# Performance work log

Measured on AMD Instinct MI355X. Metric: run time of the kernel, lower is better.

## Reference

```python
import jax, jax.numpy as jnp
import numpy as np

D_MODEL = 1024
N_HEADS = 16
D_K = D_MODEL // N_HEADS
SEQ = 2048
BATCH = 2
THETA = 10000.0


def apply_rope(x, positions, theta):
    # x: [..., h, s, d_k], positions: [s]
    d_k = x.shape[-1]
    inv_freq = 1.0 / (theta ** (jnp.arange(0, d_k, 2, dtype=jnp.float32) / d_k))  # [d_k/2]
    ang = positions.astype(jnp.float32)[:, None] * inv_freq[None, :]  # [s, d_k/2]
    cos, sin = jnp.cos(ang), jnp.sin(ang)
    xe, xo = x[..., 0::2], x[..., 1::2]
    re = xe * cos - xo * sin
    ro = xe * sin + xo * cos
    return jnp.stack([re, ro], axis=-1).reshape(x.shape)


def setup_inputs() -> dict:
    key = jax.random.key(0)
    ks = jax.random.split(key, 7)
    f = lambda k, s: jax.random.normal(k, s, dtype=jnp.float32)
    return {
        "Q": f(ks[0], (BATCH, SEQ, D_MODEL)),
        "K": f(ks[1], (BATCH, SEQ, D_MODEL)),
        "V": f(ks[2], (BATCH, SEQ, D_MODEL)),
        "w_q": f(ks[3], (D_MODEL, D_MODEL)) * 0.02,
        "w_k": f(ks[4], (D_MODEL, D_MODEL)) * 0.02,
        "w_v": f(ks[5], (D_MODEL, D_MODEL)) * 0.02,
        "w_o": f(ks[6], (D_MODEL, D_MODEL)) * 0.02,
        "mask": jnp.tril(jnp.ones((SEQ, SEQ), dtype=bool)),
        "token_positions": jnp.arange(SEQ, dtype=jnp.int32),
    }


def reference(Q, K, V, w_q, w_k, w_v, w_o, mask, token_positions):
    h, d_k = N_HEADS, D_K
    # projections: weight is [h*d_k, d_model], applied as x @ W^T
    def proj(x, w):
        y = jnp.einsum('bsd,ed->bse', x, w)
        b, s, _ = y.shape
        return y.reshape(b, s, h, d_k).transpose(0, 2, 1, 3)  # [b,h,s,d_k]
    q = proj(Q, w_q)
    k = proj(K, w_k)
    v = proj(V, w_v)
    q = apply_rope(q, token_positions, THETA)
    k = apply_rope(k, token_positions, THETA)
    scores = jnp.einsum('bhqd,bhkd->bhqk', q, k) / jnp.sqrt(jnp.float32(d_k))
    scores = jnp.where(mask, scores, -jnp.inf)
    attn = jax.nn.softmax(scores, axis=-1)
    out = jnp.einsum('bhqk,bhkd->bhqd', attn, v)
    b, _, s, _ = out.shape
    out = out.transpose(0, 2, 1, 3).reshape(b, s, h * d_k)
    return jnp.einsum('bse,de->bsd', out, w_o)
```

## Files before the change

### kernel.cpp

```cpp
#include <hip/hip_runtime.h>

#define SEQ 2048
#define BATCH 2
#define DM 1024
#define NH 16
#define DK 64
#define BH (BATCH*NH)

typedef __attribute__((ext_vector_type(8))) short bf16x8;
typedef __attribute__((ext_vector_type(4))) float f32x4;

__device__ __forceinline__ ushort f2bf(float f) {
  union { float f; unsigned u; } v; v.f = f;
  unsigned r = (v.u + 0x7fffu + ((v.u >> 16) & 1u)) >> 16;
  return (ushort)r;
}
__device__ __forceinline__ float bf2f(ushort h) {
  union { unsigned u; float f; } v; v.u = ((unsigned)h) << 16;
  return v.f;
}
__device__ __forceinline__ unsigned cvtpk(float lo, float hi) {
  unsigned r;
  asm("v_cvt_pk_bf16_f32 %0, %1, %2" : "=v"(r) : "v"(lo), "v"(hi));
  return r;
}

#define WAITV6 asm volatile("s_waitcnt vmcnt(6)" ::: "memory")
#define WAITV3 asm volatile("s_waitcnt vmcnt(3)" ::: "memory")
#define WAITV0 asm volatile("s_waitcnt vmcnt(0)" ::: "memory")
#define WAITL0 asm volatile("s_waitcnt lgkmcnt(0)" ::: "memory")
#define BARR() __builtin_amdgcn_s_barrier()

struct P4 { const float* p0; const float* p1; const float* p2; const float* p3; };
__global__ void k_castN(P4 in, ushort* __restrict__ out, int n4) {
  const float* src = (blockIdx.z == 0) ? in.p0 : (blockIdx.z == 1) ? in.p1
                    : (blockIdx.z == 2) ? in.p2 : in.p3;
  ushort* dst = out + (size_t)blockIdx.z * (size_t)n4 * 4;
  int i = blockIdx.x * blockDim.x + threadIdx.x;
  int st = gridDim.x * blockDim.x;
  for (; i < n4; i += st) {
    float4 v = reinterpret_cast<const float4*>(src)[i];
    ushort4 o;
    o.x = f2bf(v.x); o.y = f2bf(v.y); o.z = f2bf(v.z); o.w = f2bf(v.w);
    reinterpret_cast<ushort4*>(dst)[i] = o;
  }
}

__global__ void k_rope_tab(float* __restrict__ tab) {
  int id = blockIdx.x * blockDim.x + threadIdx.x;
  if (id >= SEQ * 32) return;
  int s = id >> 5, i = id & 31;
  float inv = powf(10000.f, -(float)i / 32.f);
  float ang = (float)s * inv;
  float sn, cs;
  sincosf(ang, &sn, &cs);
  tab[id * 2] = cs;
  tab[id * 2 + 1] = sn;
}

__device__ __forceinline__ void gll16(const void* g, void* l) {
  __builtin_amdgcn_global_load_lds((const __attribute__((address_space(1))) void*)g,
                                   (__attribute__((address_space(3))) void*)l, 16, 0, 0);
}

#define GSTAGE(AD, BD, kk_) do {                                               \
    _Pragma("unroll")                                                          \
    for (int i_ = 0; i_ < 4; ++i_) {                                           \
      int tt_ = i_ * 256 + tid;                                                \
      int row_ = tt_ >> 3, c_ = (tt_ & 7) ^ (row_ & 7);                        \
      gll16(Afp + (size_t)(m0 + row_) * K + (kk_) + c_ * 4,                    \
            (void*)((char*)(AD) + (i_ * 256 + w * 64) * 16));                  \
    }                                                                          \
    gll16(Bw + (size_t)(n0 + w * 16 + lrow) * K + (kk_) + lcol, (void*)((BD) + w * 512));       \
    gll16(Bw + (size_t)(n0 + 64 + w * 16 + lrow) * K + (kk_) + lcol, (void*)((BD) + 2048 + w * 512)); \
  } while (0)

#define GCOMP(AS_, BS_) do {                                                   \
    bf16x8 af[4], bfr[4];                                                      \
    _Pragma("unroll")                                                          \
    for (int i = 0; i < 4; ++i) {                                              \
      int arow_ = wr * 64 + i * 16 + l15;                                      \
      float4 u0 = *(const float4*)((const char*)(AS_) + arow_ * 128 +          \
                                   (((l4 * 2) ^ (arow_ & 7)) * 16));           \
      float4 u1 = *(const float4*)((const char*)(AS_) + arow_ * 128 +          \
                                   (((l4 * 2 + 1) ^ (arow_ & 7)) * 16));       \
      uint4 pk_;                                                               \
      pk_.x = cvtpk(u0.x, u0.y); pk_.y = cvtpk(u0.z, u0.w);                    \
      pk_.z = cvtpk(u1.x, u1.y); pk_.w = cvtpk(u1.z, u1.w);                    \
      af[i] = *(bf16x8*)&pk_;                                                  \
    }                                                                          \
    _Pragma("unroll")                                                          \
    for (int i = 0; i < 4; ++i)                                                \
      bfr[i] = *(const bf16x8*)((BS_) + (wc * 64 + i * 16 + l15) * 32 + l4 * 8);\
    _Pragma("unroll")                                                          \
    for (int mi = 0; mi < 4; ++mi)                                             \
      _Pragma("unroll")                                                        \
      for (int ni = 0; ni < 4; ++ni)                                           \
        acc[mi][ni] = __builtin_amdgcn_mfma_f32_16x16x32_bf16(af[mi], bfr[ni], acc[mi][ni], 0, 0, 0); \
  } while (0)

__global__ __launch_bounds__(256) void k_gemm_qkv(const float* __restrict__ Qf,
                                                  const float* __restrict__ Kf,
                                                  const float* __restrict__ Vf,
                                                  const ushort* __restrict__ Bw0,
                                                  ushort* __restrict__ qT,
                                                  ushort* __restrict__ kT,
                                                  ushort* __restrict__ vT,
                                                  const float* __restrict__ tab,
                                                  float qscale, int M, int N, int K) {
  const int id = blockIdx.x;
  const int mlo = id & 7, nb = (id >> 3) & 7, mhi = (id >> 6) & 3, z = id >> 8;
  const int m0 = (mhi * 8 + mlo) * 128, n0 = nb * 128;
  const float* Afp = (z == 0) ? Qf : (z == 1) ? Kf : Vf;
  const ushort* Bw = Bw0 + (size_t)z * ((size_t)N * K);
  __shared__ float As0[4096], As1[4096];
  __shared__ ushort Bs0[4096], Bs1[4096];
  const int tid = threadIdx.x;
  const int w = tid >> 6, lane = tid & 63;
  const int l15 = lane & 15, l4 = lane >> 4;
  const int wr = w >> 1, wc = w & 1;
  const int lrow = lane >> 2, lcol = (lane & 3) * 8;
  f32x4 acc[4][4] = {};
  GSTAGE(As0, Bs0, 0);
  GSTAGE(As1, Bs1, 32);
  for (int kk = 0; kk < K - 64; kk += 64) {
    WAITV6; BARR();
    GCOMP(As0, Bs0);
    WAITL0; BARR();
    GSTAGE(As0, Bs0, kk + 64);
    WAITV6; BARR();
    GCOMP(As1, Bs1);
    WAITL0; BARR();
    if (kk + 96 < K) GSTAGE(As1, Bs1, kk + 96);
  }
  WAITV6; BARR();
  GCOMP(As0, Bs0);
  WAITV0; BARR();
  GCOMP(As1, Bs1);
  if (z == 2) {
#pragma unroll
    for (int mi = 0; mi < 4; ++mi)
#pragma unroll
      for (int ni = 0; ni < 4; ++ni) {
        int row = m0 + wr * 64 + mi * 16 + l4 * 4;
        int col = n0 + wc * 64 + ni * 16 + l15;
        int bh2 = (row >> 11) * 16 + (col >> 6);
        int d = col & 63, s = row & (SEQ - 1);
        uint2 pk;
        pk.x = cvtpk(acc[mi][ni][0], acc[mi][ni][1]);
        pk.y = cvtpk(acc[mi][ni][2], acc[mi][ni][3]);
        *(uint2*)(vT + ((size_t)bh2 * 64 + d) * SEQ + s) = pk;
      }
  } else {
    const float scale = (z == 0) ? qscale : 1.0f;
    ushort* T = (z == 0) ? qT : kT;
    const bool odd = (l15 & 1);
#pragma unroll
    for (int mi = 0; mi < 4; ++mi)
#pragma unroll
      for (int ni = 0; ni < 4; ++ni)
#pragma unroll
        for (int r = 0; r < 4; ++r) {
          int row = m0 + wr * 64 + mi * 16 + l4 * 4 + r;
          int col = n0 + wc * 64 + ni * 16 + l15;
          float v = acc[mi][ni][r];
          float pv = __shfl_xor(v, 1);
          int s = row & (SEQ - 1);
          int d = col & 63;
          float2 cs = *(const float2*)(tab + ((size_t)s * 32 + (d >> 1)) * 2);
          float xe = odd ? pv : v, xo = odd ? v : pv;
          float outv = (odd ? (xe * cs.y + xo * cs.x) : (xe * cs.x - xo * cs.y)) * scale;
          int bh2 = (row >> 11) * 16 + (col >> 6);
          T[((size_t)bh2 * SEQ + s) * 64 + d] = f2bf(outv);
        }
  }
}

#define FSTAGE(AD, BD, kk_) do {                                               \
    gll16(A + (size_t)(m0 + srow) * K + (kk_) + scol, (void*)((AD) + w * 512));\
    gll16(Bw + (size_t)(n0 + srow) * K + (kk_) + scol, (void*)((BD) + w * 512));\
    gll16(Bw + (size_t)(n0 + 64 + srow) * K + (kk_) + scol, (void*)((BD) + 2048 + w * 512)); \
  } while (0)

#define FCOMP(AS_, BS_) do {                                                   \
    bf16x8 af[2], bfr[4];                                                      \
    _Pragma("unroll")                                                          \
    for (int i = 0; i < 2; ++i)                                                \
      af[i] = *(const bf16x8*)((AS_) + (wr * 32 + i * 16 + l15) * 32 + l4 * 8);\
    _Pragma("unroll")                                                          \
    for (int i = 0; i < 4; ++i)                                                \
      bfr[i] = *(const bf16x8*)((BS_) + (wc * 64 + i * 16 + l15) * 32 + l4 * 8);\
    _Pragma("unroll")                                                          \
    for (int mi = 0; mi < 2; ++mi)                                             \
      _Pragma("unroll")                                                        \
      for (int ni = 0; ni < 4; ++ni)                                           \
        acc[mi][ni] = __builtin_amdgcn_mfma_f32_16x16x32_bf16(af[mi], bfr[ni], acc[mi][ni], 0, 0, 0); \
  } while (0)

__global__ __launch_bounds__(256) void k_gemm_f(const ushort* __restrict__ A,
                                                const ushort* __restrict__ Bw,
                                                float* __restrict__ C, int M, int N, int K) {
  const int id = blockIdx.x;
  const int mlo = id & 7, nb = (id >> 3) & 7, mhi = id >> 6;
  const int m0 = (mhi * 8 + mlo) * 64, n0 = nb * 128;
  __shared__ ushort As0[64 * 32], Bs0[128 * 32];
  __shared__ ushort As1[64 * 32], Bs1[128 * 32];
  const int tid = threadIdx.x;
  const int w = tid >> 6, lane = tid & 63;
  const int l15 = lane & 15, l4 = lane >> 4;
  const int wr = w >> 1, wc = w & 1;
  const int srow = tid >> 2, scol = (tid & 3) * 8;
  f32x4 acc[2][4] = {};
  FSTAGE(As0, Bs0, 0);
  FSTAGE(As1, Bs1, 32);
  for (int kk = 0; kk < K - 64; kk += 64) {
    WAITV3; BARR();
    FCOMP(As0, Bs0);
    WAITL0; BARR();
    FSTAGE(As0, Bs0, kk + 64);
    WAITV3; BARR();
    FCOMP(As1, Bs1);
    WAITL0; BARR();
    if (kk + 96 < K) FSTAGE(As1, Bs1, kk + 96);
  }
  WAITV3; BARR();
  FCOMP(As0, Bs0);
  WAITV0; BARR();
  FCOMP(As1, Bs1);
#pragma unroll
  for (int mi = 0; mi < 2; ++mi)
#pragma unroll
    for (int ni = 0; ni < 4; ++ni)
#pragma unroll
      for (int r = 0; r < 4; ++r) {
        int row = m0 + wr * 32 + mi * 16 + l4 * 4 + r;
        int col = n0 + wc * 64 + ni * 16 + l15;
        C[(size_t)row * N + col] = acc[mi][ni][r];
      }
}

#define KSTAGE(DST, kt_) do {                                                  \
    const ushort* kb_ = kT + hb + (size_t)(kt_) * 8192;                        \
    _Pragma("unroll")                                                          \
    for (int i_ = 0; i_ < 4; ++i_) {                                           \
      int tt_ = i_ * 256 + tid;                                                \
      int row_ = tt_ >> 3, c_ = (tt_ & 7) ^ (row_ & 7);                        \
      gll16(kb_ + (size_t)row_ * 64 + c_ * 8,                                  \
            (void*)((char*)(DST) + (i_ * 256 + w * 64) * 16));                 \
    }                                                                          \
  } while (0)

#define VSTAGE(DST, kt_) do {                                                  \
    const ushort* vb_ = vT + vbase + (size_t)(kt_) * 128;                      \
    _Pragma("unroll")                                                          \
    for (int i_ = 0; i_ < 4; ++i_) {                                           \
      int tt_ = i_ * 256 + tid;                                                \
      int row_ = tt_ >> 4, c_ = (tt_ & 15) ^ (row_ & 15);                      \
      gll16(vb_ + (size_t)row_ * SEQ + c_ * 8,                                 \
            (void*)((char*)(DST) + (i_ * 256 + w * 64) * 16));                 \
    }                                                                          \
  } while (0)

#define FRK(BASE, row_, cidx)                                                  \
  (*(const bf16x8*)((const char*)(BASE) + (row_) * 128 + ((((cidx) ^ ((row_) & 7)) & 7) * 16)))
#define FRV(BASE, row_, cidx)                                                  \
  (*(const bf16x8*)((const char*)(BASE) + (row_) * 256 + ((((cidx) ^ ((row_) & 15)) & 15) * 16)))

#define SMAX8(P, MRUN, LRUN, ACC) do {                                         \
    float mx = P[0][0];                                                        \
    _Pragma("unroll")                                                          \
    for (int nf = 0; nf < 8; ++nf)                                             \
      _Pragma("unroll")                                                        \
      for (int r = 0; r < 4; ++r) mx = fmaxf(mx, P[nf][r]);                    \
    mx = fmaxf(mx, __shfl_xor(mx, 16));                                        \
    mx = fmaxf(mx, __shfl_xor(mx, 32));                                        \
    if (!__all(mx <= MRUN)) {                                                  \
      const float mn = fmaxf(MRUN, mx);                                        \
      const float so = __builtin_amdgcn_exp2f(MRUN - mn);                      \
      float soq[4];                                                            \
      _Pragma("unroll")                                                        \
      for (int r = 0; r < 4; ++r) soq[r] = __shfl(so, l4 * 4 + r);             \
      _Pragma("unroll")                                                        \
      for (int df = 0; df < 4; ++df)                                           \
        _Pragma("unroll")                                                      \
        for (int r = 0; r < 4; ++r) ACC[df][r] *= soq[r];                      \
      LRUN *= so;                                                              \
      MRUN = mn;                                                               \
    }                                                                          \
    float rs = 0.f;                                                            \
    _Pragma("unroll")                                                          \
    for (int nf = 0; nf < 8; ++nf) {                                           \
      float e0 = __builtin_amdgcn_exp2f(P[nf][0] - MRUN);                      \
      float e1 = __builtin_amdgcn_exp2f(P[nf][1] - MRUN);                      \
      float e2 = __builtin_amdgcn_exp2f(P[nf][2] - MRUN);                      \
      float e3 = __builtin_amdgcn_exp2f(P[nf][3] - MRUN);                      \
      P[nf][0] = e0; P[nf][1] = e1; P[nf][2] = e2; P[nf][3] = e3;              \
      rs += (e0 + e1) + (e2 + e3);                                             \
    }                                                                          \
    LRUN += rs;                                                                \
  } while (0)

#define PVHALF(P, MYP, ACC, VC, H) do {                                        \
    _Pragma("unroll")                                                          \
    for (int i = 0; i < 4; ++i) {                                              \
      uint2 pk;                                                                \
      pk.x = cvtpk(P[(H) * 4 + i][0], P[(H) * 4 + i][1]);                      \
      pk.y = cvtpk(P[(H) * 4 + i][2], P[(H) * 4 + i][3]);                      \
      *(uint2*)((MYP) + ((l15 * 128 + i * 32 + l4 * 8) ^ swz)) = pk;           \
    }                                                                          \
    const bf16x8 pa0 = *(const bf16x8*)((MYP) + ((l15 * 128 + l4 * 16) ^ swz));\
    const bf16x8 pa1 = *(const bf16x8*)((MYP) + ((l15 * 128 + 64 + l4 * 16) ^ swz));\
    _Pragma("unroll")                                                          \
    for (int df = 0; df < 4; ++df) {                                           \
      bf16x8 v0_ = FRV(VC, df * 16 + l15, (H) * 8 + l4);                       \
      bf16x8 v1_ = FRV(VC, df * 16 + l15, (H) * 8 + l4 + 4);                   \
      ACC[df] = __builtin_amdgcn_mfma_f32_16x16x32_bf16(pa0, v0_, ACC[df], 0, 0, 0); \
      ACC[df] = __builtin_amdgcn_mfma_f32_16x16x32_bf16(pa1, v1_, ACC[df], 0, 0, 0); \
    }                                                                          \
  } while (0)

#define STEP(KC, VC, KN, VN, kt_, DIAG, PREF) do {                             \
    if (PREF) { KSTAGE(KN, (kt_) + 1); VSTAGE(VN, (kt_) + 1); }                \
    float p0[8][4], p1[8][4];                                                  \
    _Pragma("unroll")                                                          \
    for (int nf = 0; nf < 8; ++nf) {                                           \
      bf16x8 k0_ = FRK(KC, nf * 16 + l15, l4);                                 \
      bf16x8 k1_ = FRK(KC, nf * 16 + l15, l4 + 4);                             \
      if (!(DIAG) || nf < 4) {                                                 \
        f32x4 z = {0.f, 0.f, 0.f, 0.f};                                        \
        z = __builtin_amdgcn_mfma_f32_16x16x32_bf16(k0_, qb00, z, 0, 0, 0);    \
        z = __builtin_amdgcn_mfma_f32_16x16x32_bf16(k1_, qb01, z, 0, 0, 0);    \
        _Pragma("unroll")                                                      \
        for (int r = 0; r < 4; ++r) {                                          \
          float sc = z[r];                                                     \
          if (DIAG && (nf * 16 + l4 * 4 + r) > (w * 16 + l15)) sc = -INFINITY; \
          p0[nf][r] = sc;                                                      \
        }                                                                      \
      } else {                                                                 \
        _Pragma("unroll")                                                      \
        for (int r = 0; r < 4; ++r) p0[nf][r] = -INFINITY;                     \
      }                                                                        \
      {                                                                        \
        f32x4 z = {0.f, 0.f, 0.f, 0.f};                                        \
        z = __builtin_amdgcn_mfma_f32_16x16x32_bf16(k0_, qb10, z, 0, 0, 0);    \
        z = __builtin_amdgcn_mfma_f32_16x16x32_bf16(k1_, qb11, z, 0, 0, 0);    \
        _Pragma("unroll")                                                      \
        for (int r = 0; r < 4; ++r) {                                          \
          float sc = z[r];                                                     \
          if (DIAG && (nf * 16 + l4 * 4 + r) > (64 + w * 16 + l15)) sc = -INFINITY; \
          p1[nf][r] = sc;                                                      \
        }                                                                      \
      }                                                                        \
    }                                                                          \
    SMAX8(p0, mrun0, lrun0, acc0);                                             \
    SMAX8(p1, mrun1, lrun1, acc1);                                             \
    PVHALF(p0, myP0, acc0, VC, 0);                                             \
    if (!(DIAG)) PVHALF(p0, myP0, acc0, VC, 1);                                \
    PVHALF(p1, myP1, acc1, VC, 0);                                             \
    PVHALF(p1, myP1, acc1, VC, 1);                                             \
    __syncthreads();                                                           \
  } while (0)

__global__ __launch_bounds__(256, 2) void k_flash(const ushort* __restrict__ qT,
                                                  const ushort* __restrict__ kT,
                                                  const ushort* __restrict__ vT,
                                                  ushort* __restrict__ AO) {
  __shared__ ushort Ks[2][128 * 64];
  __shared__ ushort Vs[2][64 * 128];
  __shared__ char Plds[4 * 4096];
  const int l = blockIdx.x;
  const int bh = (l & 7) * 4 + ((l >> 3) & 3);
  const int qt = (SEQ / 128 - 1) - (l >> 5);
  const int tid = threadIdx.x, w = tid >> 6, lane = tid & 63;
  const int l15 = lane & 15, l4 = lane >> 4;
  const size_t hb = (size_t)bh * SEQ * DK;
  const size_t vbase = (size_t)bh * DK * SEQ;
  const int qrow0 = qt * 128 + w * 16;
  const int qrow1 = qrow0 + 64;
  const bf16x8 qb00 = *(const bf16x8*)(qT + hb + (size_t)(qrow0 + l15) * 64 + l4 * 8);
  const bf16x8 qb01 = *(const bf16x8*)(qT + hb + (size_t)(qrow0 + l15) * 64 + 32 + l4 * 8);
  const bf16x8 qb10 = *(const bf16x8*)(qT + hb + (size_t)(qrow1 + l15) * 64 + l4 * 8);
  const bf16x8 qb11 = *(const bf16x8*)(qT + hb + (size_t)(qrow1 + l15) * 64 + 32 + l4 * 8);
  f32x4 acc0[4] = {}, acc1[4] = {};
  float mrun0 = -INFINITY, lrun0 = 0.f, mrun1 = -INFINITY, lrun1 = 0.f;
  char* myP0 = (char*)Plds + w * 4096;
  char* myP1 = myP0 + 2048;
  const int swz = (l15 & 7) << 4;
  ushort* kc = &Ks[0][0]; ushort* vc = &Vs[0][0];
  ushort* kn = &Ks[1][0]; ushort* vn = &Vs[1][0];
  KSTAGE(kc, 0); VSTAGE(vc, 0);
  __syncthreads();
  for (int kt = 0; kt < qt; ++kt) {
    STEP(kc, vc, kn, vn, kt, false, true);
    ushort* t;
    t = kc; kc = kn; kn = t;
    t = vc; vc = vn; vn = t;
  }
  STEP(kc, vc, kn, vn, qt, true, false);
  lrun0 += __shfl_xor(lrun0, 16); lrun0 += __shfl_xor(lrun0, 32);
  lrun1 += __shfl_xor(lrun1, 16); lrun1 += __shfl_xor(lrun1, 32);
  const int b = bh >> 4, h = bh & 15;
  float lq0[4], lq1[4];
#pragma unroll
  for (int r = 0; r < 4; ++r) {
    lq0[r] = __shfl(lrun0, l4 * 4 + r);
    lq1[r] = __shfl(lrun1, l4 * 4 + r);
  }
#pragma unroll
  for (int r = 0; r < 4; ++r) {
    float inv0 = 1.f / lq0[r], inv1 = 1.f / lq1[r];
    int qr0 = qrow0 + l4 * 4 + r, qr1 = qrow1 + l4 * 4 + r;
#pragma unroll
    for (int df = 0; df < 4; ++df) {
      AO[(size_t)(b * SEQ + qr0) * DM + h * 64 + df * 16 + l15] = f2bf(acc0[df][r] * inv0);
      AO[(size_t)(b * SEQ + qr1) * DM + h * 64 + df * 16 + l15] = f2bf(acc1[df][r] * inv1);
    }
  }
}

extern "C" void kernel_launch(void* const* d_in, const int* in_sizes, int n_in,
                              void* d_out, int out_size, void* d_ws, size_t ws_size,
                              hipStream_t stream) {
  const float* Q = (const float*)d_in[0];
  const float* K = (const float*)d_in[1];
  const float* V = (const float*)d_in[2];
  const float* wq = (const float*)d_in[3];
  const float* wk = (const float*)d_in[4];
  const float* wv = (const float*)d_in[5];
  const float* wo = (const float*)d_in[6];
  float* out = (float*)d_out;
  char* ws = (char*)d_ws;

  ushort* qT = (ushort*)(ws + 0);
  ushort* kT = (ushort*)(ws + 8388608);
  ushort* vT = (ushort*)(ws + 16777216);
  ushort* WQ = (ushort*)(ws + 25165824);
  ushort* AO = (ushort*)(ws + 33554432);
  float* TAB = (float*)(ws + 41943040);

  const int NW4 = DM * DM / 4;
  P4 win = {wq, wk, wv, wo};
  k_castN<<<dim3(1024, 1, 4), 256, 0, stream>>>(win, WQ, NW4);
  k_rope_tab<<<(SEQ * 32) / 256, 256, 0, stream>>>(TAB);

  const float QSCALE = 0.125f * 1.4426950408889634f;
  k_gemm_qkv<<<768, 256, 0, stream>>>(Q, K, V, WQ, qT, kT, vT, TAB, QSCALE,
                                      BATCH * SEQ, DM, DM);

  k_flash<<<BH * (SEQ / 128), 256, 0, stream>>>(qT, kT, vT, AO);

  k_gemm_f<<<512, 256, 0, stream>>>(AO, WQ + 3 * DM * DM, out, BATCH * SEQ, DM, DM);
}
```

Baseline: 129.0 us.

## Pre-cast Q/K/V activations to bf16 before the QKV projection GEMM

```diff
diff --git a/kernel.cpp b/kernel.cpp
--- a/kernel.cpp
+++ b/kernel.cpp
@@ -25,7 +25,7 @@
   return r;
 }
 
-#define WAITV6 asm volatile("s_waitcnt vmcnt(6)" ::: "memory")
+#define WAITV4 asm volatile("s_waitcnt vmcnt(4)" ::: "memory")
 #define WAITV3 asm volatile("s_waitcnt vmcnt(3)" ::: "memory")
 #define WAITV0 asm volatile("s_waitcnt vmcnt(0)" ::: "memory")
 #define WAITL0 asm volatile("s_waitcnt lgkmcnt(0)" ::: "memory")
@@ -64,13 +64,8 @@
 }
 
 #define GSTAGE(AD, BD, kk_) do {                                               \
-    _Pragma("unroll")                                                          \
-    for (int i_ = 0; i_ < 4; ++i_) {                                           \
-      int tt_ = i_ * 256 + tid;                                                \
-      int row_ = tt_ >> 3, c_ = (tt_ & 7) ^ (row_ & 7);                        \
-      gll16(Afp + (size_t)(m0 + row_) * K + (kk_) + c_ * 4,                    \
-            (void*)((char*)(AD) + (i_ * 256 + w * 64) * 16));                  \
-    }                                                                          \
+    gll16(A + (size_t)(m0 + w * 16 + lrow) * K + (kk_) + lcol, (void*)((AD) + w * 512));        \
+    gll16(A + (size_t)(m0 + 64 + w * 16 + lrow) * K + (kk_) + lcol, (void*)((AD) + 2048 + w * 512)); \
     gll16(Bw + (size_t)(n0 + w * 16 + lrow) * K + (kk_) + lcol, (void*)((BD) + w * 512));       \
     gll16(Bw + (size_t)(n0 + 64 + w * 16 + lrow) * K + (kk_) + lcol, (void*)((BD) + 2048 + w * 512)); \
   } while (0)
@@ -78,17 +73,8 @@
 #define GCOMP(AS_, BS_) do {                                                   \
     bf16x8 af[4], bfr[4];                                                      \
     _Pragma("unroll")                                                          \
-    for (int i = 0; i < 4; ++i) {                                              \
-      int arow_ = wr * 64 + i * 16 + l15;                                      \
-      float4 u0 = *(const float4*)((const char*)(AS_) + arow_ * 128 +          \
-                                   (((l4 * 2) ^ (arow_ & 7)) * 16));           \
-      float4 u1 = *(const float4*)((const char*)(AS_) + arow_ * 128 +          \
-                                   (((l4 * 2 + 1) ^ (arow_ & 7)) * 16));       \
-      uint4 pk_;                                                               \
-      pk_.x = cvtpk(u0.x, u0.y); pk_.y = cvtpk(u0.z, u0.w);                    \
-      pk_.z = cvtpk(u1.x, u1.y); pk_.w = cvtpk(u1.z, u1.w);                    \
-      af[i] = *(bf16x8*)&pk_;                                                  \
-    }                                                                          \
+    for (int i = 0; i < 4; ++i)                                                \
+      af[i] = *(const bf16x8*)((AS_) + (wr * 64 + i * 16 + l15) * 32 + l4 * 8);\
     _Pragma("unroll")                                                          \
     for (int i = 0; i < 4; ++i)                                                \
       bfr[i] = *(const bf16x8*)((BS_) + (wc * 64 + i * 16 + l15) * 32 + l4 * 8);\
@@ -99,9 +85,7 @@
         acc[mi][ni] = __builtin_amdgcn_mfma_f32_16x16x32_bf16(af[mi], bfr[ni], acc[mi][ni], 0, 0, 0); \
   } while (0)
 
-__global__ __launch_bounds__(256) void k_gemm_qkv(const float* __restrict__ Qf,
-                                                  const float* __restrict__ Kf,
-                                                  const float* __restrict__ Vf,
+__global__ __launch_bounds__(256) void k_gemm_qkv(const ushort* __restrict__ A0,
                                                   const ushort* __restrict__ Bw0,
                                                   ushort* __restrict__ qT,
                                                   ushort* __restrict__ kT,
@@ -111,10 +95,10 @@
   const int id = blockIdx.x;
   const int mlo = id & 7, nb = (id >> 3) & 7, mhi = (id >> 6) & 3, z = id >> 8;
   const int m0 = (mhi * 8 + mlo) * 128, n0 = nb * 128;
-  const float* Afp = (z == 0) ? Qf : (z == 1) ? Kf : Vf;
+  const ushort* A = A0 + (size_t)z * ((size_t)M * K);
   const ushort* Bw = Bw0 + (size_t)z * ((size_t)N * K);
-  __shared__ float As0[4096], As1[4096];
-  __shared__ ushort Bs0[4096], Bs1[4096];
+  __shared__ ushort As0[128 * 32], Bs0[128 * 32];
+  __shared__ ushort As1[128 * 32], Bs1[128 * 32];
   const int tid = threadIdx.x;
   const int w = tid >> 6, lane = tid & 63;
   const int l15 = lane & 15, l4 = lane >> 4;
@@ -124,16 +108,16 @@
   GSTAGE(As0, Bs0, 0);
   GSTAGE(As1, Bs1, 32);
   for (int kk = 0; kk < K - 64; kk += 64) {
-    WAITV6; BARR();
+    WAITV4; BARR();
     GCOMP(As0, Bs0);
     WAITL0; BARR();
     GSTAGE(As0, Bs0, kk + 64);
-    WAITV6; BARR();
+    WAITV4; BARR();
     GCOMP(As1, Bs1);
     WAITL0; BARR();
     if (kk + 96 < K) GSTAGE(As1, Bs1, kk + 96);
   }
-  WAITV6; BARR();
+  WAITV4; BARR();
   GCOMP(As0, Bs0);
   WAITV0; BARR();
   GCOMP(As1, Bs1);
@@ -431,20 +415,24 @@
   float* out = (float*)d_out;
   char* ws = (char*)d_ws;
 
-  ushort* qT = (ushort*)(ws + 0);
-  ushort* kT = (ushort*)(ws + 8388608);
-  ushort* vT = (ushort*)(ws + 16777216);
+  ushort* XQ = (ushort*)(ws + 0);
   ushort* WQ = (ushort*)(ws + 25165824);
-  ushort* AO = (ushort*)(ws + 33554432);
-  float* TAB = (float*)(ws + 41943040);
-
+  ushort* qT = (ushort*)(ws + 33554432);
+  ushort* kT = (ushort*)(ws + 41943040);
+  ushort* vT = (ushort*)(ws + 50331648);
+  float* TAB = (float*)(ws + 58720256);
+  ushort* AO = XQ;
+
+  const int NX4 = BATCH * SEQ * DM / 4;
   const int NW4 = DM * DM / 4;
+  P4 xin = {Q, K, V, nullptr};
   P4 win = {wq, wk, wv, wo};
+  k_castN<<<dim3(2048, 1, 3), 256, 0, stream>>>(xin, XQ, NX4);
   k_castN<<<dim3(1024, 1, 4), 256, 0, stream>>>(win, WQ, NW4);
   k_rope_tab<<<(SEQ * 32) / 256, 256, 0, stream>>>(TAB);
 
   const float QSCALE = 0.125f * 1.4426950408889634f;
-  k_gemm_qkv<<<768, 256, 0, stream>>>(Q, K, V, WQ, qT, kT, vT, TAB, QSCALE,
+  k_gemm_qkv<<<768, 256, 0, stream>>>(XQ, WQ, qT, kT, vT, TAB, QSCALE,
                                       BATCH * SEQ, DM, DM);
 
   k_flash<<<BH * (SEQ / 128), 256, 0, stream>>>(qT, kT, vT, AO);
```

Result: faster. 123.6 us (-4.2%).
